# Kernel tuning notes

Hardware: AMD Instinct MI355X
Metric: run time of the kernel (lower is better)

## Reference

```python
import jax, jax.numpy as jnp
import numpy as np

N_NODES = 20000


def _segment_softmax(alpha, dst, num_nodes):
    # numerically-stable softmax over edges grouped by destination node
    m = jax.ops.segment_max(alpha, dst, num_segments=num_nodes)
    m = jnp.where(jnp.isfinite(m), m, 0.0)
    a = jnp.exp(alpha - m[dst])
    denom = jax.ops.segment_sum(a, dst, num_segments=num_nodes)
    return a / denom[dst]


def mgcn_conv(x, src, dst, edge_type, basis, att, weight, root, bias, num_nodes):
    # x: [N, in], basis: [B, in, out], att: [R, B], weight: [R, out=in]
    x_i = x[dst]                                   # [E, in] target feats
    x_j = x[src]                                   # [E, in] source feats
    # per-edge attention logit: sum_d x_i[d] * w_r[d] * x_j[d]
    alpha = jnp.sum(x_i * weight[edge_type] * x_j, axis=1)   # [E]
    alpha = _segment_softmax(alpha, dst, num_nodes)          # [E]
    # basis-decomposed per-edge transform: x_j @ (att_r . basis)
    t = jnp.einsum('ei,bio->ebo', x_j, basis)                # [E, B, out]
    msg = jnp.einsum('ebo,eb->eo', t, att[edge_type])        # [E, out]
    msg = msg * alpha[:, None]
    out = jax.ops.segment_sum(msg, dst, num_segments=num_nodes)  # [N, out]
    return out + x @ root + bias


def setup_inputs() -> dict:
    key = jax.random.key(0)
    ks = jax.random.split(key, 16)
    E, D, R, B, N = 32768, 128, 474, 64, N_NODES
    s = 0.05
    return {
        'entity': jnp.arange(N, dtype=jnp.int64) if jax.config.jax_enable_x64 else jnp.arange(N, dtype=jnp.int32),
        'edge_index': jax.random.randint(ks[0], (2, E), 0, N, dtype=jnp.int32),
        'edge_type': jax.random.randint(ks[1], (E,), 0, R, dtype=jnp.int32),
        'emb_table': jax.random.normal(ks[2], (N, D), dtype=jnp.float32),
        'basis1': jax.random.normal(ks[3], (B, D, D), dtype=jnp.float32) * s,
        'att1': jax.random.normal(ks[4], (R, B), dtype=jnp.float32) * s,
        'weight1': jax.random.normal(ks[5], (R, D), dtype=jnp.float32) * s,
        'root1': jax.random.normal(ks[6], (D, D), dtype=jnp.float32) * s,
        'bias1': jnp.zeros((D,), dtype=jnp.float32),
        'basis2': jax.random.normal(ks[7], (B, D, D), dtype=jnp.float32) * s,
        'att2': jax.random.normal(ks[8], (R, B), dtype=jnp.float32) * s,
        'weight2': jax.random.normal(ks[9], (R, D), dtype=jnp.float32) * s,
        'root2': jax.random.normal(ks[10], (D, D), dtype=jnp.float32) * s,
        'bias2': jnp.zeros((D,), dtype=jnp.float32),
    }


def reference(entity, edge_index, edge_type, emb_table,
              basis1, att1, weight1, root1, bias1,
              basis2, att2, weight2, root2, bias2):
    src, dst = edge_index[0], edge_index[1]   # PyG: (source j, target i)
    x = emb_table[entity]                     # embedding lookup
    h = jax.nn.relu(mgcn_conv(x, src, dst, edge_type, basis1, att1,
                              weight1, root1, bias1, N_NODES))
    # dropout is identity at inference
    out = mgcn_conv(h, src, dst, edge_type, basis2, att2,
                    weight2, root2, bias2, N_NODES)
    return out
```

## Files before the change

kernel.cpp:

```cpp
#include <hip/hip_runtime.h>
#include <hip/hip_bf16.h>

#define N_NODES 20000
#define N_EDGES 32768
#define DIM 128
#define N_REL 474
#define N_BASIS 64
#define TILE_E 64
#define MAXCH (N_EDGES / TILE_E + N_REL)
#define WSTRIDE 264
#define HIST_BLKS 16
#define EDGES_PER_HIST (N_EDGES / HIST_BLKS)
#define WMIX_BLKS 128
#define TR_BLKS 2
#define GATHER_BASE (WMIX_BLKS + TR_BLKS)
#define LOGIT_BLKS (N_EDGES / 16)
#define ROOT_BLKS ((N_NODES + 63) / 64)

typedef __bf16 bf16x8 __attribute__((ext_vector_type(8)));
typedef float f32x4 __attribute__((ext_vector_type(4)));

__device__ __forceinline__ unsigned short f2b(float f) {
    unsigned u = __float_as_uint(f);
    unsigned r = (u + 0x7FFFu + ((u >> 16) & 1u)) >> 16;
    return (unsigned short)r;
}
__device__ __forceinline__ float b2f(unsigned short s) {
    return __uint_as_float(((unsigned)s) << 16);
}
__device__ __forceinline__ __bf16 u2b(unsigned short u) {
    union { unsigned short u; __bf16 b; } c; c.u = u; return c.b;
}
__device__ __forceinline__ int4 packrelu8(float4 a0, float4 a1) {
    int4 v;
    v.x = (int)((unsigned)f2b(fmaxf(a0.x, 0.f)) | ((unsigned)f2b(fmaxf(a0.y, 0.f)) << 16));
    v.y = (int)((unsigned)f2b(fmaxf(a0.z, 0.f)) | ((unsigned)f2b(fmaxf(a0.w, 0.f)) << 16));
    v.z = (int)((unsigned)f2b(fmaxf(a1.x, 0.f)) | ((unsigned)f2b(fmaxf(a1.y, 0.f)) << 16));
    v.w = (int)((unsigned)f2b(fmaxf(a1.z, 0.f)) | ((unsigned)f2b(fmaxf(a1.w, 0.f)) << 16));
    return v;
}
__device__ __forceinline__ float dot2bf(unsigned a, unsigned b, float wx, float wy) {
    return b2f((unsigned short)(a & 0xFFFFu)) * wx * b2f((unsigned short)(b & 0xFFFFu))
         + b2f((unsigned short)(a >> 16)) * wy * b2f((unsigned short)(b >> 16));
}

__global__ __launch_bounds__(256) void prepmix_kernel(const float4* __restrict__ emb,
                                                      const int* __restrict__ entity,
                                                      const int* __restrict__ etype,
                                                      ushort4* __restrict__ xb4,
                                                      float4* __restrict__ zreg, int zcount4,
                                                      int* __restrict__ partial,
                                                      const float* __restrict__ att1,
                                                      const float* __restrict__ basis1,
                                                      unsigned short* __restrict__ W1,
                                                      const float* __restrict__ att2,
                                                      const float* __restrict__ basis2,
                                                      unsigned short* __restrict__ W2,
                                                      const float* __restrict__ root1,
                                                      unsigned short* __restrict__ rootT1,
                                                      const float* __restrict__ root2,
                                                      unsigned short* __restrict__ rootT2) {
    __shared__ __align__(16) unsigned short bt[64 * WSTRIDE];
    int t = threadIdx.x;
    if (blockIdx.x < WMIX_BLKS) {
        int wi = blockIdx.x;
        const float* att   = (wi >= 64) ? att2 : att1;
        const float* basis = (wi >= 64) ? basis2 : basis1;
        unsigned short* W  = (wi >= 64) ? W2 : W1;
        int io0 = (wi & 63) * 256;
#pragma unroll
        for (int p = 0; p < 16; p++) {
            int c = t + 256 * p;
            int k = c >> 6, of = c & 63;
            float4 v = *(const float4*)(basis + (size_t)k * (DIM * DIM) + io0 + of * 4);
            ushort4 s;
            s.x = f2b(v.x); s.y = f2b(v.y); s.z = f2b(v.z); s.w = f2b(v.w);
            int ofx = of ^ (((k >> 3) & 7) << 2);
            *(ushort4*)&bt[k * WSTRIDE + ofx * 4] = s;
        }
        __syncthreads();

        int w = t >> 6, l = t & 63, n = l & 15, q = l >> 4;
        bf16x8 bfr[2][4];
#pragma unroll
        for (int kb = 0; kb < 2; kb++) {
            int kbase = kb * 32 + q * 8;
            int sx = ((kb * 4 + q) & 7) << 4;
#pragma unroll
            for (int c = 0; c < 4; c++) {
                int ob = (w * 64 + c * 16 + n) ^ sx;
#pragma unroll
                for (int j = 0; j < 8; j++) bfr[kb][c][j] = u2b(bt[(kbase + j) * WSTRIDE + ob]);
            }
        }
#pragma unroll 1
        for (int rg = 0; rg < 8; rg++) {
            int r0 = rg * 64;
            f32x4 acc[4][4] = {};
#pragma unroll
            for (int kb = 0; kb < 2; kb++) {
                int kbase = kb * 32 + q * 8;
                bf16x8 a[4];
#pragma unroll
                for (int rt = 0; rt < 4; rt++) {
                    int rm = min(r0 + rt * 16 + n, N_REL - 1);
                    const float4* ap = (const float4*)(att + (size_t)rm * N_BASIS + kbase);
                    float4 u0 = ap[0], u1 = ap[1];
                    a[rt][0] = (__bf16)u0.x; a[rt][1] = (__bf16)u0.y;
                    a[rt][2] = (__bf16)u0.z; a[rt][3] = (__bf16)u0.w;
                    a[rt][4] = (__bf16)u1.x; a[rt][5] = (__bf16)u1.y;
                    a[rt][6] = (__bf16)u1.z; a[rt][7] = (__bf16)u1.w;
                }
#pragma unroll
                for (int c = 0; c < 4; c++) {
#pragma unroll
                    for (int rt = 0; rt < 4; rt++)
                        acc[rt][c] = __builtin_amdgcn_mfma_f32_16x16x32_bf16(a[rt], bfr[kb][c], acc[rt][c], 0, 0, 0);
                }
            }
#pragma unroll
            for (int rt = 0; rt < 4; rt++) {
#pragma unroll
                for (int c = 0; c < 4; c++) {
                    int col = io0 + w * 64 + c * 16 + n;
#pragma unroll
                    for (int g = 0; g < 4; g++) {
                        int r = r0 + rt * 16 + q * 4 + g;
                        if (r < N_REL) W[(size_t)r * (DIM * DIM) + col] = f2b(acc[rt][c][g]);
                    }
                }
            }
        }
    } else if (blockIdx.x < GATHER_BASE) {
        int wi2 = blockIdx.x - WMIX_BLKS;
        const float* rm = wi2 ? root2 : root1;
        unsigned short* rt_ = wi2 ? rootT2 : rootT1;
        unsigned short* sb16 = bt;
#pragma unroll
        for (int p = 0; p < 16; p++) {
            int idx = t + 256 * p;
            int k = idx >> 5, o4 = idx & 31;
            float4 v = ((const float4*)rm)[idx];
            ushort4 s;
            s.x = f2b(v.x); s.y = f2b(v.y); s.z = f2b(v.z); s.w = f2b(v.w);
            *(ushort4*)&sb16[k * 132 + o4 * 4] = s;
        }
        __syncthreads();
        int o = t >> 1, kh = (t & 1) * 64;
#pragma unroll
        for (int i = 0; i < 16; i++) {
            int k0 = kh + i * 4;
            ushort4 s;
            s.x = sb16[(k0 + 0) * 132 + o];
            s.y = sb16[(k0 + 1) * 132 + o];
            s.z = sb16[(k0 + 2) * 132 + o];
            s.w = sb16[(k0 + 3) * 132 + o];
            *(ushort4*)&rt_[o * DIM + k0] = s;
        }
    } else {
        int pb = blockIdx.x - GATHER_BASE;
        int gtid = pb * 256 + t;
        int gsz = 1024 * 256;
        int total4 = N_NODES * DIM / 4;
        for (int i = gtid; i < total4; i += gsz) {
            int n = i >> 5, rem = i & 31;
            float4 v = emb[(size_t)entity[n] * 32 + rem];
            ushort4 s;
            s.x = f2b(v.x); s.y = f2b(v.y); s.z = f2b(v.z); s.w = f2b(v.w);
            xb4[i] = s;
        }
        float4 z = make_float4(0.f, 0.f, 0.f, 0.f);
        for (int i = gtid; i < zcount4; i += gsz) zreg[i] = z;
        if (pb < HIST_BLKS) {
            int* ih = (int*)bt;
            for (int i = t; i < N_REL; i += 256) ih[i] = 0;
            __syncthreads();
            int e0 = pb * EDGES_PER_HIST;
            for (int e = e0 + t; e < e0 + EDGES_PER_HIST; e += 256)
                atomicAdd(&ih[etype[e]], 1);
            __syncthreads();
            for (int i = t; i < N_REL; i += 256) partial[pb * N_REL + i] = ih[i];
        }
    }
}

__global__ void scanr_kernel(const int* __restrict__ partial, int* __restrict__ offs,
                             int* __restrict__ cursor, int* __restrict__ chunk_r,
                             int* __restrict__ chunk_o, int* __restrict__ nchunks) {
    __shared__ int s[512];
    __shared__ int lnc;
    int t = threadIdx.x;
    int v = 0;
    if (t < N_REL) {
#pragma unroll
        for (int k = 0; k < HIST_BLKS; k++) v += partial[k * N_REL + t];
    }
    s[t] = v;
    if (t == 0) lnc = 0;
    __syncthreads();
    for (int d = 1; d < 512; d <<= 1) {
        int add = (t >= d) ? s[t - d] : 0;
        __syncthreads();
        s[t] += add;
        __syncthreads();
    }
    int excl = s[t] - v;
    if (t < N_REL) { offs[t] = excl; cursor[t] = excl; }
    if (t == 0) offs[N_REL] = N_EDGES;
    if (t < N_REL && v > 0) {
        int nc = (v + TILE_E - 1) / TILE_E;
        int cb = atomicAdd(&lnc, nc);
        for (int c = 0; c < nc; c++) { chunk_r[cb + c] = t; chunk_o[cb + c] = excl + c * TILE_E; }
    }
    __syncthreads();
    if (t == 0) *nchunks = lnc;
}

__global__ __launch_bounds__(256) void fused_kernel(const unsigned short* __restrict__ xb,
                                                    const float* __restrict__ xf,
                                                    const float* __restrict__ w,
                                                    const int* __restrict__ src,
                                                    const int* __restrict__ dst,
                                                    const int* __restrict__ et,
                                                    int* __restrict__ cursor,
                                                    int* __restrict__ eids,
                                                    int do_scatter,
                                                    float* __restrict__ alpha,
                                                    float* __restrict__ den,
                                                    const unsigned short* __restrict__ rootT,
                                                    const float* __restrict__ bias,
                                                    float* __restrict__ target) {
    __shared__ __align__(16) unsigned short xrf[8192];
    int t = threadIdx.x;
    if (blockIdx.x < LOGIT_BLKS) {
        int eg = blockIdx.x * 16 + (t >> 4);
        int lane = t & 15;
        int s = src[eg], d = dst[eg], r = et[eg];
        if (do_scatter && lane == 0) {
            int p = atomicAdd(&cursor[r], 1);
            eids[p] = eg;
        }
        const float4* wp = (const float4*)(w + (size_t)r * DIM);
        float4 w0 = wp[lane * 2], w1 = wp[lane * 2 + 1];
        float v;
        if (xf == nullptr) {
            int4 av = ((const int4*)(xb + (size_t)s * DIM))[lane];
            int4 bv = ((const int4*)(xb + (size_t)d * DIM))[lane];
            v = dot2bf((unsigned)av.x, (unsigned)bv.x, w0.x, w0.y)
              + dot2bf((unsigned)av.y, (unsigned)bv.y, w0.z, w0.w)
              + dot2bf((unsigned)av.z, (unsigned)bv.z, w1.x, w1.y)
              + dot2bf((unsigned)av.w, (unsigned)bv.w, w1.z, w1.w);
        } else {
            const float4* ap = (const float4*)(xf + (size_t)s * DIM);
            const float4* bp = (const float4*)(xf + (size_t)d * DIM);
            float4 a0 = ap[lane * 2], a1 = ap[lane * 2 + 1];
            float4 b0 = bp[lane * 2], b1 = bp[lane * 2 + 1];
            v = fmaxf(a0.x, 0.f) * w0.x * fmaxf(b0.x, 0.f)
              + fmaxf(a0.y, 0.f) * w0.y * fmaxf(b0.y, 0.f)
              + fmaxf(a0.z, 0.f) * w0.z * fmaxf(b0.z, 0.f)
              + fmaxf(a0.w, 0.f) * w0.w * fmaxf(b0.w, 0.f)
              + fmaxf(a1.x, 0.f) * w1.x * fmaxf(b1.x, 0.f)
              + fmaxf(a1.y, 0.f) * w1.y * fmaxf(b1.y, 0.f)
              + fmaxf(a1.z, 0.f) * w1.z * fmaxf(b1.z, 0.f)
              + fmaxf(a1.w, 0.f) * w1.w * fmaxf(b1.w, 0.f);
        }
        v += __shfl_xor(v, 8, 64);
        v += __shfl_xor(v, 4, 64);
        v += __shfl_xor(v, 2, 64);
        v += __shfl_xor(v, 1, 64);
        if (lane == 0) {
            float a = expf(v);
            alpha[eg] = a;
            atomicAdd(&den[d], a);
        }
    } else {
        int n0 = (blockIdx.x - LOGIT_BLKS) * 64;
#pragma unroll
        for (int p = 0; p < 4; p++) {
            int c = t + 256 * p;
            int g = c >> 6;
            int rt = g >> 2, kb = g & 3;
            int q = (c >> 4) & 3, m = c & 15;
            int row = n0 + rt * 16 + m;
            int oct = kb * 4 + q;
            int4 v = make_int4(0, 0, 0, 0);
            if (row < N_NODES) {
                if (xf == nullptr) {
                    v = *(const int4*)(xb + (size_t)row * DIM + oct * 8);
                } else {
                    const float4* sp = (const float4*)(xf + (size_t)row * DIM + oct * 8);
                    v = packrelu8(sp[0], sp[1]);
                }
            }
            *(int4*)&xrf[c * 8] = v;
        }
        __syncthreads();

        int w_ = t >> 6, l = t & 63, n = l & 15, q = l >> 4;
        f32x4 acc[2][4] = {};
#pragma unroll
        for (int kb = 0; kb < 4; kb++) {
            bf16x8 a[4];
#pragma unroll
            for (int rt = 0; rt < 4; rt++) a[rt] = *(const bf16x8*)&xrf[((rt * 4 + kb) * 64 + l) * 8];
            int kbase = kb * 32 + q * 8;
#pragma unroll
            for (int c = 0; c < 2; c++) {
                int col = (w_ * 2 + c) * 16 + n;
                bf16x8 b = *(const bf16x8*)(rootT + (size_t)col * DIM + kbase);
#pragma unroll
                for (int rt = 0; rt < 4; rt++)
                    acc[c][rt] = __builtin_amdgcn_mfma_f32_16x16x32_bf16(a[rt], b, acc[c][rt], 0, 0, 0);
            }
        }
#pragma unroll
        for (int c = 0; c < 2; c++) {
            int col = (w_ * 2 + c) * 16 + n;
            float bo = bias[col];
#pragma unroll
            for (int rt = 0; rt < 4; rt++) {
#pragma unroll
                for (int rg = 0; rg < 4; rg++) {
                    int row = n0 + rt * 16 + q * 4 + rg;
                    if (row < N_NODES)
                        target[(size_t)row * DIM + col] = acc[c][rt][rg] + bo;
                }
            }
        }
    }
}

__global__ __launch_bounds__(256) void msg_kernel(const unsigned short* __restrict__ xb,
                                                  const float* __restrict__ xf,
                                                  const unsigned short* __restrict__ W,
                                                  const int* __restrict__ chunk_r,
                                                  const int* __restrict__ chunk_off,
                                                  const int* __restrict__ nchunks,
                                                  const int* __restrict__ eids,
                                                  const int* __restrict__ offs,
                                                  const int* __restrict__ src,
                                                  const int* __restrict__ dst,
                                                  const float* __restrict__ ae,
                                                  const float* __restrict__ denom,
                                                  float* __restrict__ outacc) {
    if ((int)blockIdx.x >= *nchunks) return;
    int r = chunk_r[blockIdx.x];
    int base = chunk_off[blockIdx.x];
    int nE = min(TILE_E, offs[r + 1] - base);
    const unsigned short* Wr = W + (size_t)r * (DIM * DIM);

    __shared__ __align__(16) unsigned short wt[128 * 136];
    __shared__ __align__(16) unsigned short xjf[8192];
    __shared__ float scf[TILE_E];
    __shared__ int sdd[TILE_E];

    int t = threadIdx.x;
    if (t < TILE_E) {
        if (t < nE) {
            int e = eids[base + t];
            int d_ = dst[e];
            sdd[t] = d_;
            scf[t] = ae[e] / denom[d_];
        } else { sdd[t] = 0; scf[t] = 0.f; }
    }
#pragma unroll
    for (int p = 0; p < 4; p++) {
        int c = t + 256 * p;
        int g = c >> 6;
        int rt = g >> 2, kb = g & 3;
        int q = (c >> 4) & 3, m = c & 15;
        int e = rt * 16 + m;
        int oct = kb * 4 + q;
        int4 v = make_int4(0, 0, 0, 0);
        if (e < nE) {
            size_t rowoff = (size_t)src[eids[base + e]] * DIM + oct * 8;
            if (xf == nullptr) {
                v = *(const int4*)(xb + rowoff);
            } else {
                const float4* sp = (const float4*)(xf + rowoff);
                v = packrelu8(sp[0], sp[1]);
            }
        }
        *(int4*)&xjf[c * 8] = v;
    }
#pragma unroll
    for (int p = 0; p < 8; p++) {
        int c = t + 256 * p;
        int k = c >> 4, oct = c & 15;
        int4 v = *(const int4*)(Wr + k * DIM + oct * 8);
        int oct2 = oct ^ (((k >> 3) & 7) << 1);
        *(int4*)&wt[k * 136 + oct2 * 8] = v;
    }
    __syncthreads();

    int w = t >> 6, l = t & 63, n = l & 15, q = l >> 4;
    f32x4 acc[2][4] = {};
#pragma unroll
    for (int kb = 0; kb < 4; kb++) {
        bf16x8 a[4];
#pragma unroll
        for (int rt = 0; rt < 4; rt++) a[rt] = *(const bf16x8*)&xjf[((rt * 4 + kb) * 64 + l) * 8];
        int kbase = kb * 32 + q * 8;
        int sx = ((kb * 4 + q) & 7) << 4;
#pragma unroll
        for (int c = 0; c < 2; c++) {
            int ob = ((w * 2 + c) * 16 + n) ^ sx;
            bf16x8 b;
#pragma unroll
            for (int j = 0; j < 8; j++) b[j] = u2b(wt[(kbase + j) * 136 + ob]);
#pragma unroll
            for (int rt = 0; rt < 4; rt++)
                acc[c][rt] = __builtin_amdgcn_mfma_f32_16x16x32_bf16(a[rt], b, acc[c][rt], 0, 0, 0);
        }
    }
#pragma unroll
    for (int c = 0; c < 2; c++) {
        int col = (w * 2 + c) * 16 + n;
#pragma unroll
        for (int rt = 0; rt < 4; rt++) {
#pragma unroll
            for (int rg = 0; rg < 4; rg++) {
                int e = rt * 16 + q * 4 + rg;
                if (e < nE)
                    atomicAdd(&outacc[(size_t)sdd[e] * DIM + col], scf[e] * acc[c][rt][rg]);
            }
        }
    }
}

extern "C" void kernel_launch(void* const* d_in, const int* in_sizes, int n_in,
                              void* d_out, int out_size, void* d_ws, size_t ws_size,
                              hipStream_t stream) {
    const int N = N_NODES, E = N_EDGES, R = N_REL;

    const int* entity = (const int*)d_in[0];
    const int* eidx   = (const int*)d_in[1];
    const int* src    = eidx;
    const int* dst    = eidx + E;
    const int* etype  = (const int*)d_in[2];
    const float* emb  = (const float*)d_in[3];
    const float* basis1 = (const float*)d_in[4];
    const float* att1   = (const float*)d_in[5];
    const float* w1     = (const float*)d_in[6];
    const float* root1  = (const float*)d_in[7];
    const float* bias1  = (const float*)d_in[8];
    const float* basis2 = (const float*)d_in[9];
    const float* att2   = (const float*)d_in[10];
    const float* w2     = (const float*)d_in[11];
    const float* root2  = (const float*)d_in[12];
    const float* bias2  = (const float*)d_in[13];
    float* out = (float*)d_out;

    size_t off = 0;
    auto alloc = [&](size_t bytes) -> void* {
        void* p = (char*)d_ws + off;
        off += (bytes + 255) & ~(size_t)255;
        return p;
    };
    unsigned short* W1 = (unsigned short*)alloc((size_t)R * DIM * DIM * 2);
    unsigned short* W2 = (unsigned short*)alloc((size_t)R * DIM * DIM * 2);
    unsigned short* xb = (unsigned short*)alloc((size_t)N * DIM * 2);
    float* acc1   = (float*)alloc((size_t)N * DIM * 4);
    float* zreg   = (float*)alloc((size_t)2 * N * 4);
    float* denom1 = zreg;
    float* denom2 = zreg + N;
    float* alpha  = (float*)alloc((size_t)E * 4);
    int* partial  = (int*)alloc((size_t)HIST_BLKS * R * 4);
    int* nchunks  = (int*)alloc(256);
    int* offs     = (int*)alloc((size_t)(R + 1) * 4);
    int* cursor   = (int*)alloc((size_t)R * 4);
    int* eids     = (int*)alloc((size_t)E * 4);
    int* chunk_r  = (int*)alloc((size_t)MAXCH * 4);
    int* chunk_o  = (int*)alloc((size_t)MAXCH * 4);
    unsigned short* rootT1 = (unsigned short*)alloc((size_t)DIM * DIM * 2);
    unsigned short* rootT2 = (unsigned short*)alloc((size_t)DIM * DIM * 2);

    int zcount4 = 2 * N / 4;

    prepmix_kernel<<<GATHER_BASE + 1024, 256, 0, stream>>>((const float4*)emb, entity, etype,
                                             (ushort4*)xb, (float4*)zreg, zcount4, partial,
                                             att1, basis1, W1, att2, basis2, W2,
                                             root1, rootT1, root2, rootT2);
    scanr_kernel<<<1, 512, 0, stream>>>(partial, offs, cursor, chunk_r, chunk_o, nchunks);

    fused_kernel<<<LOGIT_BLKS + ROOT_BLKS, 256, 0, stream>>>(
        xb, nullptr, w1, src, dst, etype, cursor, eids, 1, alpha, denom1, rootT1, bias1, acc1);
    msg_kernel<<<MAXCH, 256, 0, stream>>>(xb, nullptr, W1, chunk_r, chunk_o, nchunks,
                                          eids, offs, src, dst, alpha, denom1, acc1);

    fused_kernel<<<LOGIT_BLKS + ROOT_BLKS, 256, 0, stream>>>(
        nullptr, acc1, w2, src, dst, etype, cursor, eids, 0, alpha, denom2, rootT2, bias2, out);
    msg_kernel<<<MAXCH, 256, 0, stream>>>(nullptr, acc1, W2, chunk_r, chunk_o, nchunks,
                                          eids, offs, src, dst, alpha, denom2, out);
}
```

Baseline: 220.8 us.

## Replace relation sort with per-relation block edge scan and deferred softmax normalization

Drops the histogram, scan and scatter kernels. Each msg_kernel block now handles one relation: it scans all edge types with ballot compaction into a shared edge list, computes the attention logits inline, and accumulates unnormalized messages and denominators with atomics. A new fin_kernel divides by the denominator and adds the root transform and bias, writing layer-1 output as bf16 with ReLU applied. This cuts kernel launches and intermediate traffic, but every block reads the full edge-type array, a relation with more than 1024 edges would be silently truncated, and zeroing now covers two N×D float accumulators.

After: 227.9 us. +3.2%, slower.

```diff
diff --git a/kernel.cpp b/kernel.cpp
--- a/kernel.cpp
+++ b/kernel.cpp
@@ -7,15 +7,12 @@
 #define N_REL 474
 #define N_BASIS 64
 #define TILE_E 64
-#define MAXCH (N_EDGES / TILE_E + N_REL)
 #define WSTRIDE 264
-#define HIST_BLKS 16
-#define EDGES_PER_HIST (N_EDGES / HIST_BLKS)
 #define WMIX_BLKS 128
 #define TR_BLKS 2
 #define GATHER_BASE (WMIX_BLKS + TR_BLKS)
-#define LOGIT_BLKS (N_EDGES / 16)
-#define ROOT_BLKS ((N_NODES + 63) / 64)
+#define FIN_BLKS ((N_NODES + 63) / 64)
+#define LELIST 1024
 
 typedef __bf16 bf16x8 __attribute__((ext_vector_type(8)));
 typedef float f32x4 __attribute__((ext_vector_type(4)));
@@ -31,35 +28,25 @@
 __device__ __forceinline__ __bf16 u2b(unsigned short u) {
     union { unsigned short u; __bf16 b; } c; c.u = u; return c.b;
 }
-__device__ __forceinline__ int4 packrelu8(float4 a0, float4 a1) {
-    int4 v;
-    v.x = (int)((unsigned)f2b(fmaxf(a0.x, 0.f)) | ((unsigned)f2b(fmaxf(a0.y, 0.f)) << 16));
-    v.y = (int)((unsigned)f2b(fmaxf(a0.z, 0.f)) | ((unsigned)f2b(fmaxf(a0.w, 0.f)) << 16));
-    v.z = (int)((unsigned)f2b(fmaxf(a1.x, 0.f)) | ((unsigned)f2b(fmaxf(a1.y, 0.f)) << 16));
-    v.w = (int)((unsigned)f2b(fmaxf(a1.z, 0.f)) | ((unsigned)f2b(fmaxf(a1.w, 0.f)) << 16));
-    return v;
-}
 __device__ __forceinline__ float dot2bf(unsigned a, unsigned b, float wx, float wy) {
     return b2f((unsigned short)(a & 0xFFFFu)) * wx * b2f((unsigned short)(b & 0xFFFFu))
          + b2f((unsigned short)(a >> 16)) * wy * b2f((unsigned short)(b >> 16));
 }
 
-__global__ __launch_bounds__(256) void prepmix_kernel(const float4* __restrict__ emb,
-                                                      const int* __restrict__ entity,
-                                                      const int* __restrict__ etype,
-                                                      ushort4* __restrict__ xb4,
-                                                      float4* __restrict__ zreg, int zcount4,
-                                                      int* __restrict__ partial,
-                                                      const float* __restrict__ att1,
-                                                      const float* __restrict__ basis1,
-                                                      unsigned short* __restrict__ W1,
-                                                      const float* __restrict__ att2,
-                                                      const float* __restrict__ basis2,
-                                                      unsigned short* __restrict__ W2,
-                                                      const float* __restrict__ root1,
-                                                      unsigned short* __restrict__ rootT1,
-                                                      const float* __restrict__ root2,
-                                                      unsigned short* __restrict__ rootT2) {
+__global__ __launch_bounds__(256) void prep_kernel(const float4* __restrict__ emb,
+                                                   const int* __restrict__ entity,
+                                                   ushort4* __restrict__ xb4,
+                                                   float4* __restrict__ zreg, int zcount4,
+                                                   const float* __restrict__ att1,
+                                                   const float* __restrict__ basis1,
+                                                   unsigned short* __restrict__ W1,
+                                                   const float* __restrict__ att2,
+                                                   const float* __restrict__ basis2,
+                                                   unsigned short* __restrict__ W2,
+                                                   const float* __restrict__ root1,
+                                                   unsigned short* __restrict__ rootT1,
+                                                   const float* __restrict__ root2,
+                                                   unsigned short* __restrict__ rootT2) {
     __shared__ __align__(16) unsigned short bt[64 * WSTRIDE];
     int t = threadIdx.x;
     if (blockIdx.x < WMIX_BLKS) {
@@ -171,218 +158,31 @@
         }
         float4 z = make_float4(0.f, 0.f, 0.f, 0.f);
         for (int i = gtid; i < zcount4; i += gsz) zreg[i] = z;
-        if (pb < HIST_BLKS) {
-            int* ih = (int*)bt;
-            for (int i = t; i < N_REL; i += 256) ih[i] = 0;
-            __syncthreads();
-            int e0 = pb * EDGES_PER_HIST;
-            for (int e = e0 + t; e < e0 + EDGES_PER_HIST; e += 256)
-                atomicAdd(&ih[etype[e]], 1);
-            __syncthreads();
-            for (int i = t; i < N_REL; i += 256) partial[pb * N_REL + i] = ih[i];
-        }
-    }
-}
-
-__global__ void scanr_kernel(const int* __restrict__ partial, int* __restrict__ offs,
-                             int* __restrict__ cursor, int* __restrict__ chunk_r,
-                             int* __restrict__ chunk_o, int* __restrict__ nchunks) {
-    __shared__ int s[512];
-    __shared__ int lnc;
-    int t = threadIdx.x;
-    int v = 0;
-    if (t < N_REL) {
-#pragma unroll
-        for (int k = 0; k < HIST_BLKS; k++) v += partial[k * N_REL + t];
-    }
-    s[t] = v;
-    if (t == 0) lnc = 0;
-    __syncthreads();
-    for (int d = 1; d < 512; d <<= 1) {
-        int add = (t >= d) ? s[t - d] : 0;
-        __syncthreads();
-        s[t] += add;
-        __syncthreads();
-    }
-    int excl = s[t] - v;
-    if (t < N_REL) { offs[t] = excl; cursor[t] = excl; }
-    if (t == 0) offs[N_REL] = N_EDGES;
-    if (t < N_REL && v > 0) {
-        int nc = (v + TILE_E - 1) / TILE_E;
-        int cb = atomicAdd(&lnc, nc);
-        for (int c = 0; c < nc; c++) { chunk_r[cb + c] = t; chunk_o[cb + c] = excl + c * TILE_E; }
-    }
-    __syncthreads();
-    if (t == 0) *nchunks = lnc;
-}
-
-__global__ __launch_bounds__(256) void fused_kernel(const unsigned short* __restrict__ xb,
-                                                    const float* __restrict__ xf,
-                                                    const float* __restrict__ w,
-                                                    const int* __restrict__ src,
-                                                    const int* __restrict__ dst,
-                                                    const int* __restrict__ et,
-                                                    int* __restrict__ cursor,
-                                                    int* __restrict__ eids,
-                                                    int do_scatter,
-                                                    float* __restrict__ alpha,
-                                                    float* __restrict__ den,
-                                                    const unsigned short* __restrict__ rootT,
-                                                    const float* __restrict__ bias,
-                                                    float* __restrict__ target) {
-    __shared__ __align__(16) unsigned short xrf[8192];
-    int t = threadIdx.x;
-    if (blockIdx.x < LOGIT_BLKS) {
-        int eg = blockIdx.x * 16 + (t >> 4);
-        int lane = t & 15;
-        int s = src[eg], d = dst[eg], r = et[eg];
-        if (do_scatter && lane == 0) {
-            int p = atomicAdd(&cursor[r], 1);
-            eids[p] = eg;
-        }
-        const float4* wp = (const float4*)(w + (size_t)r * DIM);
-        float4 w0 = wp[lane * 2], w1 = wp[lane * 2 + 1];
-        float v;
-        if (xf == nullptr) {
-            int4 av = ((const int4*)(xb + (size_t)s * DIM))[lane];
-            int4 bv = ((const int4*)(xb + (size_t)d * DIM))[lane];
-            v = dot2bf((unsigned)av.x, (unsigned)bv.x, w0.x, w0.y)
-              + dot2bf((unsigned)av.y, (unsigned)bv.y, w0.z, w0.w)
-              + dot2bf((unsigned)av.z, (unsigned)bv.z, w1.x, w1.y)
-              + dot2bf((unsigned)av.w, (unsigned)bv.w, w1.z, w1.w);
-        } else {
-            const float4* ap = (const float4*)(xf + (size_t)s * DIM);
-            const float4* bp = (const float4*)(xf + (size_t)d * DIM);
-            float4 a0 = ap[lane * 2], a1 = ap[lane * 2 + 1];
-            float4 b0 = bp[lane * 2], b1 = bp[lane * 2 + 1];
-            v = fmaxf(a0.x, 0.f) * w0.x * fmaxf(b0.x, 0.f)
-              + fmaxf(a0.y, 0.f) * w0.y * fmaxf(b0.y, 0.f)
-              + fmaxf(a0.z, 0.f) * w0.z * fmaxf(b0.z, 0.f)
-              + fmaxf(a0.w, 0.f) * w0.w * fmaxf(b0.w, 0.f)
-              + fmaxf(a1.x, 0.f) * w1.x * fmaxf(b1.x, 0.f)
-              + fmaxf(a1.y, 0.f) * w1.y * fmaxf(b1.y, 0.f)
-              + fmaxf(a1.z, 0.f) * w1.z * fmaxf(b1.z, 0.f)
-              + fmaxf(a1.w, 0.f) * w1.w * fmaxf(b1.w, 0.f);
-        }
-        v += __shfl_xor(v, 8, 64);
-        v += __shfl_xor(v, 4, 64);
-        v += __shfl_xor(v, 2, 64);
-        v += __shfl_xor(v, 1, 64);
-        if (lane == 0) {
-            float a = expf(v);
-            alpha[eg] = a;
-            atomicAdd(&den[d], a);
-        }
-    } else {
-        int n0 = (blockIdx.x - LOGIT_BLKS) * 64;
-#pragma unroll
-        for (int p = 0; p < 4; p++) {
-            int c = t + 256 * p;
-            int g = c >> 6;
-            int rt = g >> 2, kb = g & 3;
-            int q = (c >> 4) & 3, m = c & 15;
-            int row = n0 + rt * 16 + m;
-            int oct = kb * 4 + q;
-            int4 v = make_int4(0, 0, 0, 0);
-            if (row < N_NODES) {
-                if (xf == nullptr) {
-                    v = *(const int4*)(xb + (size_t)row * DIM + oct * 8);
-                } else {
-                    const float4* sp = (const float4*)(xf + (size_t)row * DIM + oct * 8);
-                    v = packrelu8(sp[0], sp[1]);
-                }
-            }
-            *(int4*)&xrf[c * 8] = v;
-        }
-        __syncthreads();
-
-        int w_ = t >> 6, l = t & 63, n = l & 15, q = l >> 4;
-        f32x4 acc[2][4] = {};
-#pragma unroll
-        for (int kb = 0; kb < 4; kb++) {
-            bf16x8 a[4];
-#pragma unroll
-            for (int rt = 0; rt < 4; rt++) a[rt] = *(const bf16x8*)&xrf[((rt * 4 + kb) * 64 + l) * 8];
-            int kbase = kb * 32 + q * 8;
-#pragma unroll
-            for (int c = 0; c < 2; c++) {
-                int col = (w_ * 2 + c) * 16 + n;
-                bf16x8 b = *(const bf16x8*)(rootT + (size_t)col * DIM + kbase);
-#pragma unroll
-                for (int rt = 0; rt < 4; rt++)
-                    acc[c][rt] = __builtin_amdgcn_mfma_f32_16x16x32_bf16(a[rt], b, acc[c][rt], 0, 0, 0);
-            }
-        }
-#pragma unroll
-        for (int c = 0; c < 2; c++) {
-            int col = (w_ * 2 + c) * 16 + n;
-            float bo = bias[col];
-#pragma unroll
-            for (int rt = 0; rt < 4; rt++) {
-#pragma unroll
-                for (int rg = 0; rg < 4; rg++) {
-                    int row = n0 + rt * 16 + q * 4 + rg;
-                    if (row < N_NODES)
-                        target[(size_t)row * DIM + col] = acc[c][rt][rg] + bo;
-                }
-            }
-        }
     }
 }
 
 __global__ __launch_bounds__(256) void msg_kernel(const unsigned short* __restrict__ xb,
-                                                  const float* __restrict__ xf,
                                                   const unsigned short* __restrict__ W,
-                                                  const int* __restrict__ chunk_r,
-                                                  const int* __restrict__ chunk_off,
-                                                  const int* __restrict__ nchunks,
-                                                  const int* __restrict__ eids,
-                                                  const int* __restrict__ offs,
+                                                  const float* __restrict__ wlog,
                                                   const int* __restrict__ src,
                                                   const int* __restrict__ dst,
-                                                  const float* __restrict__ ae,
-                                                  const float* __restrict__ denom,
-                                                  float* __restrict__ outacc) {
-    if ((int)blockIdx.x >= *nchunks) return;
-    int r = chunk_r[blockIdx.x];
-    int base = chunk_off[blockIdx.x];
-    int nE = min(TILE_E, offs[r + 1] - base);
+                                                  const int* __restrict__ etype,
+                                                  float* __restrict__ den,
+                                                  float* __restrict__ accm) {
+    int r = blockIdx.x;
     const unsigned short* Wr = W + (size_t)r * (DIM * DIM);
 
     __shared__ __align__(16) unsigned short wt[128 * 136];
     __shared__ __align__(16) unsigned short xjf[8192];
+    __shared__ __align__(16) float wf[DIM];
     __shared__ float scf[TILE_E];
     __shared__ int sdd[TILE_E];
+    __shared__ int ssrc[TILE_E];
+    __shared__ int elist[LELIST];
+    __shared__ int lcnt;
 
     int t = threadIdx.x;
-    if (t < TILE_E) {
-        if (t < nE) {
-            int e = eids[base + t];
-            int d_ = dst[e];
-            sdd[t] = d_;
-            scf[t] = ae[e] / denom[d_];
-        } else { sdd[t] = 0; scf[t] = 0.f; }
-    }
-#pragma unroll
-    for (int p = 0; p < 4; p++) {
-        int c = t + 256 * p;
-        int g = c >> 6;
-        int rt = g >> 2, kb = g & 3;
-        int q = (c >> 4) & 3, m = c & 15;
-        int e = rt * 16 + m;
-        int oct = kb * 4 + q;
-        int4 v = make_int4(0, 0, 0, 0);
-        if (e < nE) {
-            size_t rowoff = (size_t)src[eids[base + e]] * DIM + oct * 8;
-            if (xf == nullptr) {
-                v = *(const int4*)(xb + rowoff);
-            } else {
-                const float4* sp = (const float4*)(xf + rowoff);
-                v = packrelu8(sp[0], sp[1]);
-            }
-        }
-        *(int4*)&xjf[c * 8] = v;
-    }
+    if (t == 0) lcnt = 0;
 #pragma unroll
     for (int p = 0; p < 8; p++) {
         int c = t + 256 * p;
@@ -391,23 +191,161 @@
         int oct2 = oct ^ (((k >> 3) & 7) << 1);
         *(int4*)&wt[k * 136 + oct2 * 8] = v;
     }
+    if (t < 32) ((float4*)wf)[t] = ((const float4*)(wlog + (size_t)r * DIM))[t];
     __syncthreads();
 
+    int lane = t & 63;
+    for (int it = 0; it < N_EDGES / 1024; it++) {
+        int idx = it * 256 + t;
+        int4 ev = ((const int4*)etype)[idx];
+#pragma unroll
+        for (int j = 0; j < 4; j++) {
+            int etj = (j == 0) ? ev.x : (j == 1) ? ev.y : (j == 2) ? ev.z : ev.w;
+            bool m = (etj == r);
+            unsigned long long bal = __ballot(m);
+            int tot = __popcll(bal);
+            if (tot) {
+                int base = 0;
+                if (lane == 0) base = atomicAdd(&lcnt, tot);
+                base = __shfl(base, 0, 64);
+                if (m) {
+                    int pre = __popcll(bal & ((1ull << lane) - 1ull));
+                    int p_ = base + pre;
+                    if (p_ < LELIST) elist[p_] = idx * 4 + j;
+                }
+            }
+        }
+    }
+    __syncthreads();
+    int cnt = min(lcnt, LELIST);
+    if (cnt == 0) return;
+
     int w = t >> 6, l = t & 63, n = l & 15, q = l >> 4;
+    int el4 = t >> 2, l4 = t & 3;
+
+    for (int t0 = 0; t0 < cnt; t0 += TILE_E) {
+        int nE = min(TILE_E, cnt - t0);
+        if (t < TILE_E) {
+            if (t < nE) {
+                int e = elist[t0 + t];
+                ssrc[t] = src[e];
+                sdd[t]  = dst[e];
+            } else { ssrc[t] = 0; sdd[t] = 0; }
+        }
+        __syncthreads();
+
+        {
+            int s_ = ssrc[el4], d_ = sdd[el4];
+            const int4* xj = (const int4*)(xb + (size_t)s_ * DIM) + l4 * 4;
+            const int4* xi = (const int4*)(xb + (size_t)d_ * DIM) + l4 * 4;
+            const float4* wv = (const float4*)&wf[l4 * 32];
+            float v = 0.f;
+#pragma unroll
+            for (int u = 0; u < 4; u++) {
+                int4 a = xj[u]; int4 b = xi[u];
+                float4 w0 = wv[u * 2], w1 = wv[u * 2 + 1];
+                v += dot2bf((unsigned)a.x, (unsigned)b.x, w0.x, w0.y)
+                   + dot2bf((unsigned)a.y, (unsigned)b.y, w0.z, w0.w)
+                   + dot2bf((unsigned)a.z, (unsigned)b.z, w1.x, w1.y)
+                   + dot2bf((unsigned)a.w, (unsigned)b.w, w1.z, w1.w);
+            }
+            v += __shfl_xor(v, 1, 64);
+            v += __shfl_xor(v, 2, 64);
+            if (l4 == 0) {
+                if (el4 < nE) {
+                    float a = expf(v);
+                    scf[el4] = a;
+                    atomicAdd(&den[d_], a);
+                } else scf[el4] = 0.f;
+            }
+        }
+
+#pragma unroll
+        for (int p = 0; p < 4; p++) {
+            int c = t + 256 * p;
+            int g = c >> 6;
+            int rt = g >> 2, kb = g & 3;
+            int q2 = (c >> 4) & 3, m = c & 15;
+            int e = rt * 16 + m;
+            int oct = kb * 4 + q2;
+            int4 v = make_int4(0, 0, 0, 0);
+            if (e < nE) v = *(const int4*)(xb + (size_t)ssrc[e] * DIM + oct * 8);
+            *(int4*)&xjf[c * 8] = v;
+        }
+        __syncthreads();
+
+        f32x4 acc[2][4] = {};
+#pragma unroll
+        for (int kb = 0; kb < 4; kb++) {
+            bf16x8 a[4];
+#pragma unroll
+            for (int rt = 0; rt < 4; rt++) a[rt] = *(const bf16x8*)&xjf[((rt * 4 + kb) * 64 + l) * 8];
+            int kbase = kb * 32 + q * 8;
+            int sx = ((kb * 4 + q) & 7) << 4;
+#pragma unroll
+            for (int c = 0; c < 2; c++) {
+                int ob = ((w * 2 + c) * 16 + n) ^ sx;
+                bf16x8 b;
+#pragma unroll
+                for (int j = 0; j < 8; j++) b[j] = u2b(wt[(kbase + j) * 136 + ob]);
+#pragma unroll
+                for (int rt = 0; rt < 4; rt++)
+                    acc[c][rt] = __builtin_amdgcn_mfma_f32_16x16x32_bf16(a[rt], b, acc[c][rt], 0, 0, 0);
+            }
+        }
+#pragma unroll
+        for (int c = 0; c < 2; c++) {
+            int col = (w * 2 + c) * 16 + n;
+#pragma unroll
+            for (int rt = 0; rt < 4; rt++) {
+#pragma unroll
+                for (int rg = 0; rg < 4; rg++) {
+                    int e = rt * 16 + q * 4 + rg;
+                    if (e < nE)
+                        atomicAdd(&accm[(size_t)sdd[e] * DIM + col], scf[e] * acc[c][rt][rg]);
+                }
+            }
+        }
+        __syncthreads();
+    }
+}
+
+__global__ __launch_bounds__(256) void fin_kernel(const unsigned short* __restrict__ xb,
+                                                  const unsigned short* __restrict__ rootT,
+                                                  const float* __restrict__ bias,
+                                                  const float* __restrict__ accm,
+                                                  const float* __restrict__ den,
+                                                  float* __restrict__ outf,
+                                                  unsigned short* __restrict__ outb) {
+    __shared__ __align__(16) unsigned short xrf[8192];
+    int t = threadIdx.x;
+    int n0 = blockIdx.x * 64;
+#pragma unroll
+    for (int p = 0; p < 4; p++) {
+        int c = t + 256 * p;
+        int g = c >> 6;
+        int rt = g >> 2, kb = g & 3;
+        int q = (c >> 4) & 3, m = c & 15;
+        int row = n0 + rt * 16 + m;
+        int oct = kb * 4 + q;
+        int4 v = make_int4(0, 0, 0, 0);
+        if (row < N_NODES) v = *(const int4*)(xb + (size_t)row * DIM + oct * 8);
+        *(int4*)&xrf[c * 8] = v;
+    }
+    __syncthreads();
+
+    int w_ = t >> 6, l = t & 63, n = l & 15, q = l >> 4;
     f32x4 acc[2][4] = {};
 #pragma unroll
     for (int kb = 0; kb < 4; kb++) {
         bf16x8 a[4];
 #pragma unroll
-        for (int rt = 0; rt < 4; rt++) a[rt] = *(const bf16x8*)&xjf[((rt * 4 + kb) * 64 + l) * 8];
+        for (int rt = 0; rt < 4; rt++) a[rt] = *(const bf16x8*)&xrf[((rt * 4 + kb) * 64 + l) * 8];
         int kbase = kb * 32 + q * 8;
-        int sx = ((kb * 4 + q) & 7) << 4;
 #pragma unroll
         for (int c = 0; c < 2; c++) {
-            int ob = ((w * 2 + c) * 16 + n) ^ sx;
-            bf16x8 b;
-#pragma unroll
-            for (int j = 0; j < 8; j++) b[j] = u2b(wt[(kbase + j) * 136 + ob]);
+            int col = (w_ * 2 + c) * 16 + n;
+            bf16x8 b = *(const bf16x8*)(rootT + (size_t)col * DIM + kbase);
 #pragma unroll
             for (int rt = 0; rt < 4; rt++)
                 acc[c][rt] = __builtin_amdgcn_mfma_f32_16x16x32_bf16(a[rt], b, acc[c][rt], 0, 0, 0);
@@ -415,14 +353,20 @@
     }
 #pragma unroll
     for (int c = 0; c < 2; c++) {
-        int col = (w * 2 + c) * 16 + n;
+        int col = (w_ * 2 + c) * 16 + n;
+        float bo = bias[col];
 #pragma unroll
         for (int rt = 0; rt < 4; rt++) {
 #pragma unroll
             for (int rg = 0; rg < 4; rg++) {
-                int e = rt * 16 + q * 4 + rg;
-                if (e < nE)
-                    atomicAdd(&outacc[(size_t)sdd[e] * DIM + col], scf[e] * acc[c][rt][rg]);
+                int row = n0 + rt * 16 + q * 4 + rg;
+                if (row < N_NODES) {
+                    float dv = den[row];
+                    float mv = accm[(size_t)row * DIM + col];
+                    float val = acc[c][rt][rg] + bo + (dv > 0.f ? mv / dv : 0.f);
+                    if (outb) outb[(size_t)row * DIM + col] = f2b(fmaxf(val, 0.f));
+                    else      outf[(size_t)row * DIM + col] = val;
+                }
             }
         }
     }
@@ -460,36 +404,24 @@
     unsigned short* W1 = (unsigned short*)alloc((size_t)R * DIM * DIM * 2);
     unsigned short* W2 = (unsigned short*)alloc((size_t)R * DIM * DIM * 2);
     unsigned short* xb = (unsigned short*)alloc((size_t)N * DIM * 2);
-    float* acc1   = (float*)alloc((size_t)N * DIM * 4);
-    float* zreg   = (float*)alloc((size_t)2 * N * 4);
-    float* denom1 = zreg;
-    float* denom2 = zreg + N;
-    float* alpha  = (float*)alloc((size_t)E * 4);
-    int* partial  = (int*)alloc((size_t)HIST_BLKS * R * 4);
-    int* nchunks  = (int*)alloc(256);
-    int* offs     = (int*)alloc((size_t)(R + 1) * 4);
-    int* cursor   = (int*)alloc((size_t)R * 4);
-    int* eids     = (int*)alloc((size_t)E * 4);
-    int* chunk_r  = (int*)alloc((size_t)MAXCH * 4);
-    int* chunk_o  = (int*)alloc((size_t)MAXCH * 4);
+    unsigned short* hb = (unsigned short*)alloc((size_t)N * DIM * 2);
+    float* zreg   = (float*)alloc(((size_t)2 * N + (size_t)2 * N * DIM) * 4);
+    float* den1   = zreg;
+    float* den2   = zreg + N;
+    float* accm1  = zreg + 2 * N;
+    float* accm2  = zreg + 2 * N + (size_t)N * DIM;
     unsigned short* rootT1 = (unsigned short*)alloc((size_t)DIM * DIM * 2);
     unsigned short* rootT2 = (unsigned short*)alloc((size_t)DIM * DIM * 2);
 
-    int zcount4 = 2 * N / 4;
-
-    prepmix_kernel<<<GATHER_BASE + 1024, 256, 0, stream>>>((const float4*)emb, entity, etype,
-                                             (ushort4*)xb, (float4*)zreg, zcount4, partial,
-                                             att1, basis1, W1, att2, basis2, W2,
-                                             root1, rootT1, root2, rootT2);
-    scanr_kernel<<<1, 512, 0, stream>>>(partial, offs, cursor, chunk_r, chunk_o, nchunks);
-
-    fused_kernel<<<LOGIT_BLKS + ROOT_BLKS, 256, 0, stream>>>(
-        xb, nullptr, w1, src, dst, etype, cursor, eids, 1, alpha, denom1, rootT1, bias1, acc1);
-    msg_kernel<<<MAXCH, 256, 0, stream>>>(xb, nullptr, W1, chunk_r, chunk_o, nchunks,
-                                          eids, offs, src, dst, alpha, denom1, acc1);
-
-    fused_kernel<<<LOGIT_BLKS + ROOT_BLKS, 256, 0, stream>>>(
-        nullptr, acc1, w2, src, dst, etype, cursor, eids, 0, alpha, denom2, rootT2, bias2, out);
-    msg_kernel<<<MAXCH, 256, 0, stream>>>(nullptr, acc1, W2, chunk_r, chunk_o, nchunks,
-                                          eids, offs, src, dst, alpha, denom2, out);
-}
+    int zcount4 = (2 * N + 2 * N * DIM) / 4;
+
+    prep_kernel<<<GATHER_BASE + 1024, 256, 0, stream>>>(
+        (const float4*)emb, entity, (ushort4*)xb, (float4*)zreg, zcount4,
+        att1, basis1, W1, att2, basis2, W2, root1, rootT1, root2, rootT2);
+
+    msg_kernel<<<N_REL, 256, 0, stream>>>(xb, W1, w1, src, dst, etype, den1, accm1);
+    fin_kernel<<<FIN_BLKS, 256, 0, stream>>>(xb, rootT1, bias1, accm1, den1, nullptr, hb);
+
+    msg_kernel<<<N_REL, 256, 0, stream>>>(hb, W2, w2, src, dst, etype, den2, accm2);
+    fin_kernel<<<FIN_BLKS, 256, 0, stream>>>(hb, rootT2, bias2, accm2, den2, out, nullptr);
+}
```
